# Optimization experiments

Measured on AMD Instinct MI355X. Metric: run time of the kernel, lower is better.

Reference implementation:

```python
import jax, jax.numpy as jnp
import numpy as np

B, T, V, H = 64, 101, 8000, 512
P_DROP = 0.3
EPS = 1e-5


def setup_inputs() -> dict:
    key = jax.random.key(0)
    ks = jax.random.split(key, 20)
    s = 1.0 / np.sqrt(H)
    inp = {
        "x": jax.random.randint(ks[0], (B, T), 0, V),
        "emb": jax.random.normal(ks[1], (V, H), jnp.float32) * 0.1,
        "Wd": jax.random.normal(ks[2], (V, H), jnp.float32) * s,
        "bd": jnp.zeros((V,), jnp.float32),
    }
    for l in range(1, 4):
        k = jax.random.split(ks[2 + l], 4)
        inp[f"Wih{l}"] = jax.random.normal(k[0], (4 * H, H), jnp.float32) * s
        inp[f"Whh{l}"] = jax.random.normal(k[1], (4 * H, H), jnp.float32) * s
        inp[f"b{l}"] = jnp.zeros((4 * H,), jnp.float32)
        inp[f"gamma{l}"] = jnp.ones((H,), jnp.float32)
        inp[f"beta{l}"] = jnp.zeros((H,), jnp.float32)
        # LockedDropout: one mask per sequence, reused at every timestep
        keep = jax.random.bernoulli(k[2], 1.0 - P_DROP, (B, H))
        inp[f"mask{l}"] = keep.astype(jnp.float32) / (1.0 - P_DROP)
    return inp


def _lstm_cell(x, h, c, Wih, Whh, b):
    gates = x @ Wih.T + h @ Whh.T + b  # [B, 4H]
    i, f, g, o = jnp.split(gates, 4, axis=-1)
    c = jax.nn.sigmoid(f) * c + jax.nn.sigmoid(i) * jnp.tanh(g)
    h = jax.nn.sigmoid(o) * jnp.tanh(c)
    return h, c


def _bn_train(h, gamma, beta):
    mu = jnp.mean(h, axis=0)
    var = jnp.mean(jnp.square(h - mu), axis=0)  # biased, as BatchNorm1d train
    return gamma * (h - mu) * jax.lax.rsqrt(var + EPS) + beta


def reference(x, emb, Wd, bd,
              Wih1, Whh1, b1, gamma1, beta1, mask1,
              Wih2, Whh2, b2, gamma2, beta2, mask2,
              Wih3, Whh3, b3, gamma3, beta3, mask3):
    e = emb[x]                      # [B, T, H]
    xs = jnp.swapaxes(e[:, :-1, :], 0, 1)  # [T-1, B, H]
    z = jnp.zeros((B, H), jnp.float32)

    def step(carry, xt):
        h1, c1, h2, c2, h3, c3 = carry
        h1, c1 = _lstm_cell(xt, h1, c1, Wih1, Whh1, b1)
        h = _bn_train(h1, gamma1, beta1) * mask1
        h2, c2 = _lstm_cell(h, h2, c2, Wih2, Whh2, b2)
        h = _bn_train(h2, gamma2, beta2) * mask2
        h3, c3 = _lstm_cell(h, h3, c3, Wih3, Whh3, b3)
        h = _bn_train(h3, gamma3, beta3) * mask3
        logits = h @ Wd.T + bd      # [B, V]
        return (h1, c1, h2, c2, h3, c3), logits

    _, logits = jax.lax.scan(step, (z, z, z, z, z, z), xs)  # [T-1, B, V]

    target_prediction = jnp.swapaxes(logits, 0, 1).reshape(-1, V)  # [B*(T-1), V]
    target = x[:, 1:].reshape(-1)
    logp = jax.nn.log_softmax(target_prediction, axis=-1)
    loss = -jnp.mean(jnp.take_along_axis(logp, target[:, None], axis=1))
    outputs = jnp.transpose(logits, (1, 2, 0))  # [B, V, T-1]
    return loss, outputs
```

## Files before the change

kernel.cpp:

```cpp
#include <hip/hip_runtime.h>
#include <hip/hip_bf16.h>
#include <math.h>

#define NBATCH 64
#define TT 101
#define TM 100
#define VV 8000
#define HH 512
#define H4 2048
#define EPSBN 1e-5f

typedef __attribute__((ext_vector_type(8))) short short8;
typedef __attribute__((ext_vector_type(4))) float floatx4;
typedef unsigned short bfraw;

__device__ __forceinline__ bfraw f2b(float f) {
  __hip_bfloat16 h = __float2bfloat16(f);
  return __builtin_bit_cast(bfraw, h);
}
__device__ __forceinline__ float sigm(float x) { return 1.f / (1.f + expf(-x)); }

__device__ __forceinline__ void st_u32_coh(bfraw* p, unsigned v) {
  __hip_atomic_store((unsigned*)p, v, __ATOMIC_RELAXED, __HIP_MEMORY_SCOPE_AGENT);
}
__device__ __forceinline__ void wait_ge(unsigned* p, unsigned target) {
  while (__hip_atomic_load(p, __ATOMIC_RELAXED, __HIP_MEMORY_SCOPE_AGENT) < target)
    __builtin_amdgcn_s_sleep(2);
}
__device__ __forceinline__ void wait_both(unsigned* p1, unsigned n1,
                                          unsigned* p2, unsigned n2) {
  for (;;) {
    unsigned a = __hip_atomic_load(p1, __ATOMIC_RELAXED, __HIP_MEMORY_SCOPE_AGENT);
    unsigned b = __hip_atomic_load(p2, __ATOMIC_RELAXED, __HIP_MEMORY_SCOPE_AGENT);
    if (a >= n1 && b >= n2) break;
    __builtin_amdgcn_s_sleep(2);
  }
}

#define GLD4(dst, base, OFFS) \
  asm volatile("global_load_dwordx4 %0, %1, off offset:" OFFS " sc1" \
               : "=&v"(dst) : "v"(base))
#define LD16(a, base) do { \
  GLD4(a[0],  base, "0");   GLD4(a[1],  base, "64");  \
  GLD4(a[2],  base, "128"); GLD4(a[3],  base, "192"); \
  GLD4(a[4],  base, "256"); GLD4(a[5],  base, "320"); \
  GLD4(a[6],  base, "384"); GLD4(a[7],  base, "448"); \
  GLD4(a[8],  base, "512"); GLD4(a[9],  base, "576"); \
  GLD4(a[10], base, "640"); GLD4(a[11], base, "704"); \
  GLD4(a[12], base, "768"); GLD4(a[13], base, "832"); \
  GLD4(a[14], base, "896"); GLD4(a[15], base, "960"); \
} while (0)

#define OFF_XE    0UL
#define OFF_X1    6553600UL
#define OFF_W1I   58982400UL
#define OFF_W1H   61079552UL
#define OFF_W2I   63176704UL
#define OFF_W2H   65273856UL
#define OFF_W3I   67371008UL
#define OFF_W3H   69468160UL
#define OFF_WDB   71565312UL
#define OFF_OUT1  79757312UL
#define OFF_OUT2  86310912UL
#define OFF_H3O   92864512UL
#define OFF_HST   99418112UL
#define OFF_ODONE 99811328UL
#define OFF_CST   100204544UL
#define OFF_SYNC  100597760UL
#define OFF_DONE  100597824UL
#define OFF_PMAX  100599040UL
#define OFF_PSUM  103799040UL
#define OFF_TLG   106999040UL

__global__ void k_zero(unsigned* p, int n) {
  int i = blockIdx.x * 256 + threadIdx.x;
  if (i < n) p[i] = 0u;
}

__global__ void k_embed(const int* __restrict__ x, const float* __restrict__ emb,
                        bfraw* __restrict__ xe) {
  int t = blockIdx.x >> 6, b = blockIdx.x & 63;
  int idx = x[b * TT + t];
  const float* src = emb + (size_t)idx * HH;
  bfraw* dst = xe + (size_t)blockIdx.x * HH;
  for (int e = threadIdx.x; e < HH; e += 256) dst[e] = f2b(src[e]);
}

__global__ void k_cast(const float* __restrict__ s, bfraw* __restrict__ d, int n) {
  int i = blockIdx.x * 256 + threadIdx.x;
  if (i < n) d[i] = f2b(s[i]);
}

__global__ __launch_bounds__(256) void k_gemm_x1(const bfraw* __restrict__ A,
                                                 const bfraw* __restrict__ Bw,
                                                 const float* __restrict__ bias,
                                                 float* __restrict__ X1) {
  int nb = blockIdx.x, mb = blockIdx.y;
  int tid = threadIdx.x, lane = tid & 63, wv = tid >> 6;
  int l15 = lane & 15, lq = lane >> 4;
  int m0 = mb * 64, n0 = nb * 64;
  floatx4 acc[4];
  for (int nt = 0; nt < 4; nt++) {
    float bv = bias[n0 + nt * 16 + l15];
    floatx4 t = {bv, bv, bv, bv};
    acc[nt] = t;
  }
  int arow = m0 + wv * 16 + l15;
  for (int ks = 0; ks < 16; ++ks) {
    int k = ks * 32 + lq * 8;
    short8 a = *(const short8*)&A[(size_t)arow * HH + k];
#pragma unroll
    for (int nt = 0; nt < 4; nt++) {
      short8 b = *(const short8*)&Bw[(size_t)(n0 + nt * 16 + l15) * HH + k];
      acc[nt] = __builtin_amdgcn_mfma_f32_16x16x32_bf16(a, b, acc[nt], 0, 0, 0);
    }
  }
#pragma unroll
  for (int nt = 0; nt < 4; nt++)
#pragma unroll
    for (int q = 0; q < 4; q++) {
      int m = m0 + wv * 16 + lq * 4 + q;
      X1[(size_t)m * H4 + n0 + nt * 16 + l15] = acc[nt][q];
    }
}

__global__ __launch_bounds__(256, 1) void k_recurrent(
    const float* __restrict__ X1,
    const bfraw* __restrict__ w1h, const bfraw* __restrict__ w2i, const bfraw* __restrict__ w2h,
    const bfraw* __restrict__ w3i, const bfraw* __restrict__ w3h,
    const float* __restrict__ b2, const float* __restrict__ b3,
    const float* __restrict__ g1, const float* __restrict__ be1, const float* __restrict__ mk1,
    const float* __restrict__ g2, const float* __restrict__ be2, const float* __restrict__ mk2,
    const float* __restrict__ g3, const float* __restrict__ be3, const float* __restrict__ mk3,
    bfraw* __restrict__ out1, bfraw* __restrict__ out2, bfraw* __restrict__ h3out,
    bfraw* __restrict__ hst, float* __restrict__ cst,
    unsigned* hdone, unsigned* odone) {
  __shared__ __align__(16) bfraw wlds[64 * 520];
  __shared__ __align__(16) float gd[64 * 65];
  __shared__ float stats[32];

  const int bid = blockIdx.x, tid = threadIdx.x;
  const int lane = tid & 63, wv = tid >> 6;
  const int l15 = lane & 15, lq = lane >> 4;

  int layer, cshift, j0;
  if (bid < 32)       { layer = 0; cshift = 4; j0 = bid << 4; }
  else if (bid < 96)  { layer = 1; cshift = 3; j0 = (bid - 32) << 3; }
  else                { layer = 2; cshift = 3; j0 = (bid - 96) << 3; }
  const int cols = 1 << cshift;
  const int NT = (layer == 0) ? 4 : 2;
  const int gstride = 4 * cols + 1;

  const bfraw* wih = (layer == 1) ? w2i : w3i;
  const bfraw* whh = (layer == 0) ? w1h : ((layer == 1) ? w2h : w3h);

  if (layer == 0) {
    for (int r = wv * 16; r < wv * 16 + 16; ++r) {
      int g = r >> 4, jj = r & 15;
      const bfraw* src = whh + (size_t)(g * HH + j0 + jj) * HH;
      *(short8*)&wlds[r * 520 + lane * 8] = *(const short8*)&src[lane * 8];
    }
  } else {
    for (int r2 = wv * 16; r2 < wv * 16 + 16; ++r2) {
      int mat = r2 >> 5, r = r2 & 31;
      int g = r >> 3, jj = r & 7;
      const bfraw* src = (mat ? whh : wih) + (size_t)(g * HH + j0 + jj) * HH;
      *(short8*)&wlds[r2 * 520 + lane * 8] = *(const short8*)&src[lane * 8];
    }
  }
  __syncthreads();

  const float* bb  = (layer == 1) ? b2 : b3;
  const float* gam = (layer == 0) ? g1 : ((layer == 1) ? g2 : g3);
  const float* bet = (layer == 0) ? be1 : ((layer == 1) ? be2 : be3);
  const float* msk = (layer == 0) ? mk1 : ((layer == 1) ? mk2 : mk3);
  bfraw* hbase = hst + (size_t)layer * 2 * NBATCH * HH;
  float* myc = cst + (size_t)layer * NBATCH * HH;

  const unsigned nprev = (layer == 1) ? 32u : 64u;
  const unsigned nself = (layer == 0) ? 32u : 64u;
  unsigned* oprev = odone + (layer - 1) * TM;
  unsigned* hself = hdone + layer * TM;
  unsigned* oself = odone + layer * TM;

  for (int t = 0; t < TM; ++t) {
    const bfraw* hr = hbase + (size_t)(t & 1) * NBATCH * HH;
    bfraw* hw = hbase + (size_t)((t + 1) & 1) * NBATCH * HH;
    const bfraw* xin = ((layer == 1) ? out1 : out2) + (size_t)t * NBATCH * HH;

    floatx4 acc[4];
    if (layer == 0) {
      const float* xrow = X1 + (size_t)t * NBATCH * H4;
      int rbase = wv * 16 + lq * 4;
#pragma unroll
      for (int nt = 0; nt < 4; nt++) {
        int colg = nt * HH + j0 + l15;
        acc[nt][0] = xrow[(rbase + 0) * H4 + colg];
        acc[nt][1] = xrow[(rbase + 1) * H4 + colg];
        acc[nt][2] = xrow[(rbase + 2) * H4 + colg];
        acc[nt][3] = xrow[(rbase + 3) * H4 + colg];
      }
    } else {
      floatx4 z = {0.f, 0.f, 0.f, 0.f};
      for (int nt = 0; nt < 4; nt++) acc[nt] = z;
    }

    if (tid == 0) {
      if (layer == 0) {
        if (t > 0) wait_ge(hself + t - 1, nself);
      } else {
        if (t > 0) wait_both(oprev + t, nprev, hself + t - 1, nself);
        else       wait_ge(oprev + t, nprev);
      }
    }
    __syncthreads();

    const int arow = wv * 16 + l15;
    const bfraw* ph = hr + (size_t)arow * HH + lq * 8;
    short8 hg[16];
    LD16(hg, ph);
    short8 xg[16];
    if (layer > 0) {
      const bfraw* px = xin + (size_t)arow * HH + lq * 8;
      LD16(xg, px);
    }
    asm volatile("s_waitcnt vmcnt(0)" ::: "memory");
    __builtin_amdgcn_sched_barrier(0);

    if (layer == 0) {
#pragma unroll
      for (int ks = 0; ks < 16; ++ks) {
        int k = ks * 32 + lq * 8;
#pragma unroll
        for (int nt = 0; nt < 4; nt++) {
          short8 bh = *(const short8*)&wlds[(nt * 16 + l15) * 520 + k];
          acc[nt] = __builtin_amdgcn_mfma_f32_16x16x32_bf16(hg[ks], bh, acc[nt], 0, 0, 0);
        }
      }
    } else {
#pragma unroll
      for (int ks = 0; ks < 16; ++ks) {
        int k = ks * 32 + lq * 8;
#pragma unroll
        for (int nt = 0; nt < 2; nt++) {
          short8 bx = *(const short8*)&wlds[(nt * 16 + l15) * 520 + k];
          short8 bh = *(const short8*)&wlds[((32 + nt * 16) + l15) * 520 + k];
          acc[nt] = __builtin_amdgcn_mfma_f32_16x16x32_bf16(xg[ks], bx, acc[nt], 0, 0, 0);
          acc[nt] = __builtin_amdgcn_mfma_f32_16x16x32_bf16(hg[ks], bh, acc[nt], 0, 0, 0);
        }
      }
    }
    {
      int rbase = wv * 16 + lq * 4;
      for (int nt = 0; nt < NT; nt++)
#pragma unroll
        for (int q = 0; q < 4; q++)
          gd[(rbase + q) * gstride + nt * 16 + l15] = acc[nt][q];
    }
    __syncthreads();
    const int half = cshift - 1;
    const int ne2 = NBATCH << half;
    for (int e = tid; e < ne2; e += 256) {
      int m = e >> half;
      int jp = (e & ((cols >> 1) - 1)) << 1;
      float hv[2];
#pragma unroll
      for (int u = 0; u < 2; u++) {
        int jj = jp + u, j = j0 + jj;
        float gi = gd[m * gstride + 0 * cols + jj];
        float gf = gd[m * gstride + 1 * cols + jj];
        float gg = gd[m * gstride + 2 * cols + jj];
        float go = gd[m * gstride + 3 * cols + jj];
        if (layer) { gi += bb[j]; gf += bb[HH + j]; gg += bb[2 * HH + j]; go += bb[3 * HH + j]; }
        float c = sigm(gf) * myc[m * HH + j] + sigm(gi) * tanhf(gg);
        float h = sigm(go) * tanhf(c);
        myc[m * HH + j] = c;
        hv[u] = h;
      }
      unsigned hpack = (unsigned)f2b(hv[0]) | ((unsigned)f2b(hv[1]) << 16);
      st_u32_coh(&hw[m * HH + j0 + jp], hpack);
      gd[m * gstride + jp] = hv[0];
      gd[m * gstride + jp + 1] = hv[1];
    }
    __builtin_amdgcn_s_waitcnt(0);
    __syncthreads();
    if (tid == 0)
      __hip_atomic_fetch_add(hself + t, 1u, __ATOMIC_RELAXED, __HIP_MEMORY_SCOPE_AGENT);
    {
      int tpc = 256 >> cshift;
      int c_ = tid >> (8 - cshift), r_ = tid & (tpc - 1);
      float s1 = 0.f, s2 = 0.f;
      for (int m = r_; m < NBATCH; m += tpc) {
        float v = gd[m * gstride + c_];
        s1 += v; s2 += v * v;
      }
      for (int off = 1; off < tpc; off <<= 1) {
        s1 += __shfl_xor(s1, off);
        s2 += __shfl_xor(s2, off);
      }
      if (r_ == 0) {
        float mu = s1 * (1.f / NBATCH);
        float var = s2 * (1.f / NBATCH) - mu * mu;
        stats[c_ * 2] = mu;
        stats[c_ * 2 + 1] = rsqrtf(var + EPSBN);
      }
    }
    __syncthreads();
    for (int e = tid; e < ne2; e += 256) {
      int m = e >> half;
      int jp = (e & ((cols >> 1) - 1)) << 1;
      float ov[2];
#pragma unroll
      for (int u = 0; u < 2; u++) {
        int jj = jp + u, j = j0 + jj;
        float h = gd[m * gstride + jj];
        ov[u] = (gam[j] * ((h - stats[jj * 2]) * stats[jj * 2 + 1]) + bet[j]) * msk[m * HH + j];
      }
      unsigned opack = (unsigned)f2b(ov[0]) | ((unsigned)f2b(ov[1]) << 16);
      if (layer == 0)
        st_u32_coh(&out1[(size_t)(t * NBATCH + m) * HH + j0 + jp], opack);
      else if (layer == 1)
        st_u32_coh(&out2[(size_t)(t * NBATCH + m) * HH + j0 + jp], opack);
      else
        *(unsigned*)&h3out[((size_t)m * TM + t) * HH + j0 + jp] = opack;
    }
    if (layer < 2) {
      __builtin_amdgcn_s_waitcnt(0);
      __syncthreads();
      if (tid == 0)
        __hip_atomic_fetch_add(oself + t, 1u, __ATOMIC_RELAXED, __HIP_MEMORY_SCOPE_AGENT);
    }
  }
}

__global__ __launch_bounds__(256) void k_dec(const bfraw* __restrict__ A,
                                             const bfraw* __restrict__ Bw,
                                             const float* __restrict__ bd,
                                             const int* __restrict__ x,
                                             float* __restrict__ out,
                                             float* __restrict__ pmax,
                                             float* __restrict__ psum,
                                             float* __restrict__ tlg) {
  __shared__ __align__(16) float tb[64 * 65];
  int nb = blockIdx.x, mb = blockIdx.y;
  int tid = threadIdx.x, lane = tid & 63, wv = tid >> 6;
  int l15 = lane & 15, lq = lane >> 4;
  int m0 = mb * 64, n0 = nb * 64;
  floatx4 acc[4];
  for (int nt = 0; nt < 4; nt++) {
    float bv = bd[n0 + nt * 16 + l15];
    floatx4 t = {bv, bv, bv, bv};
    acc[nt] = t;
  }
  int arow = m0 + wv * 16 + l15;
  for (int ks = 0; ks < 16; ++ks) {
    int k = ks * 32 + lq * 8;
    short8 a = *(const short8*)&A[(size_t)arow * HH + k];
#pragma unroll
    for (int nt = 0; nt < 4; nt++) {
      short8 b = *(const short8*)&Bw[(size_t)(n0 + nt * 16 + l15) * HH + k];
      acc[nt] = __builtin_amdgcn_mfma_f32_16x16x32_bf16(a, b, acc[nt], 0, 0, 0);
    }
  }
#pragma unroll
  for (int q = 0; q < 4; q++) {
    float mx = fmaxf(fmaxf(acc[0][q], acc[1][q]), fmaxf(acc[2][q], acc[3][q]));
    for (int off = 1; off < 16; off <<= 1) mx = fmaxf(mx, __shfl_xor(mx, off));
    float sm = expf(acc[0][q] - mx) + expf(acc[1][q] - mx) +
               expf(acc[2][q] - mx) + expf(acc[3][q] - mx);
    for (int off = 1; off < 16; off <<= 1) sm += __shfl_xor(sm, off);
    if (l15 == 0) {
      int m = m0 + wv * 16 + lq * 4 + q;
      pmax[(size_t)m * 125 + nb] = mx;
      psum[(size_t)m * 125 + nb] = sm;
    }
  }
  {
    int rbase = wv * 16 + lq * 4;
#pragma unroll
    for (int nt = 0; nt < 4; nt++)
#pragma unroll
      for (int q = 0; q < 4; q++)
        tb[(rbase + q) * 65 + nt * 16 + l15] = acc[nt][q];
  }
  __syncthreads();
  int ml = tid & 63, vq = tid >> 6;
  int m = m0 + ml;
  int b = m / TM, t = m - b * TM;
  int tgt = x[b * TT + t + 1];
  float* obase = out + (size_t)b * VV * TM + t;
  for (int i = 0; i < 16; ++i) {
    int cv = vq * 16 + i;
    int v = n0 + cv;
    float val = tb[ml * 65 + cv];
    obase[(size_t)v * TM] = val;
    if (v == tgt) tlg[m] = val;
  }
}

__global__ void k_loss(const float* __restrict__ pmax, const float* __restrict__ psum,
                       const float* __restrict__ tlg, float* acc) {
  int m = blockIdx.x * 4 + (threadIdx.x >> 6);
  int lane = threadIdx.x & 63;
  float mx = -3.4e38f;
  for (int i = lane; i < 125; i += 64) mx = fmaxf(mx, pmax[(size_t)m * 125 + i]);
  for (int off = 1; off < 64; off <<= 1) mx = fmaxf(mx, __shfl_xor(mx, off));
  float s = 0.f;
  for (int i = lane; i < 125; i += 64)
    s += psum[(size_t)m * 125 + i] * expf(pmax[(size_t)m * 125 + i] - mx);
  for (int off = 1; off < 64; off <<= 1) s += __shfl_xor(s, off);
  if (lane == 0) atomicAdd(acc, mx + logf(s) - tlg[m]);
}

__global__ void k_final(const float* acc, float* out) { out[0] = acc[0] * (1.f / 6400.f); }

extern "C" void kernel_launch(void* const* d_in, const int* in_sizes, int n_in,
                              void* d_out, int out_size, void* d_ws, size_t ws_size,
                              hipStream_t stream) {
  (void)in_sizes; (void)n_in; (void)out_size; (void)ws_size;
  const int*   x    = (const int*)  d_in[0];
  const float* emb  = (const float*)d_in[1];
  const float* Wd   = (const float*)d_in[2];
  const float* bd   = (const float*)d_in[3];
  const float* Wih1 = (const float*)d_in[4];
  const float* Whh1 = (const float*)d_in[5];
  const float* b1   = (const float*)d_in[6];
  const float* g1   = (const float*)d_in[7];
  const float* be1  = (const float*)d_in[8];
  const float* mk1  = (const float*)d_in[9];
  const float* Wih2 = (const float*)d_in[10];
  const float* Whh2 = (const float*)d_in[11];
  const float* b2   = (const float*)d_in[12];
  const float* g2   = (const float*)d_in[13];
  const float* be2  = (const float*)d_in[14];
  const float* mk2  = (const float*)d_in[15];
  const float* Wih3 = (const float*)d_in[16];
  const float* Whh3 = (const float*)d_in[17];
  const float* b3   = (const float*)d_in[18];
  const float* g3   = (const float*)d_in[19];
  const float* be3  = (const float*)d_in[20];
  const float* mk3  = (const float*)d_in[21];

  char* ws = (char*)d_ws;
  bfraw* XE   = (bfraw*)(ws + OFF_XE);
  float* X1   = (float*)(ws + OFF_X1);
  bfraw* W1I  = (bfraw*)(ws + OFF_W1I);
  bfraw* W1H  = (bfraw*)(ws + OFF_W1H);
  bfraw* W2I  = (bfraw*)(ws + OFF_W2I);
  bfraw* W2H  = (bfraw*)(ws + OFF_W2H);
  bfraw* W3I  = (bfraw*)(ws + OFF_W3I);
  bfraw* W3H  = (bfraw*)(ws + OFF_W3H);
  bfraw* WDB  = (bfraw*)(ws + OFF_WDB);
  bfraw* OUT1 = (bfraw*)(ws + OFF_OUT1);
  bfraw* OUT2 = (bfraw*)(ws + OFF_OUT2);
  bfraw* H3O  = (bfraw*)(ws + OFF_H3O);
  bfraw* HST  = (bfraw*)(ws + OFF_HST);
  float* CST  = (float*)(ws + OFF_CST);
  float* LACC = (float*)(ws + OFF_SYNC);
  unsigned* HDONE = (unsigned*)(ws + OFF_DONE);
  unsigned* ODONE = (unsigned*)(ws + OFF_ODONE);
  float* PMAX = (float*)(ws + OFF_PMAX);
  float* PSUM = (float*)(ws + OFF_PSUM);
  float* TLG  = (float*)(ws + OFF_TLG);

  int zwords = (int)((OFF_PMAX - OFF_HST) / 4);
  k_zero<<<(zwords + 255) / 256, 256, 0, stream>>>((unsigned*)(ws + OFF_HST), zwords);

  k_embed<<<6400, 256, 0, stream>>>(x, emb, XE);

  const int nw = H4 * HH;
  k_cast<<<(nw + 255) / 256, 256, 0, stream>>>(Wih1, W1I, nw);
  k_cast<<<(nw + 255) / 256, 256, 0, stream>>>(Whh1, W1H, nw);
  k_cast<<<(nw + 255) / 256, 256, 0, stream>>>(Wih2, W2I, nw);
  k_cast<<<(nw + 255) / 256, 256, 0, stream>>>(Whh2, W2H, nw);
  k_cast<<<(nw + 255) / 256, 256, 0, stream>>>(Wih3, W3I, nw);
  k_cast<<<(nw + 255) / 256, 256, 0, stream>>>(Whh3, W3H, nw);
  const int nwd = VV * HH;
  k_cast<<<(nwd + 255) / 256, 256, 0, stream>>>(Wd, WDB, nwd);

  k_gemm_x1<<<dim3(32, 100), 256, 0, stream>>>(XE, W1I, b1, X1);

  k_recurrent<<<160, 256, 0, stream>>>(X1, W1H, W2I, W2H, W3I, W3H, b2, b3,
                                       g1, be1, mk1, g2, be2, mk2, g3, be3, mk3,
                                       OUT1, OUT2, H3O, HST, CST, HDONE, ODONE);

  k_dec<<<dim3(125, 100), 256, 0, stream>>>(H3O, WDB, bd, x, ((float*)d_out) + 1,
                                            PMAX, PSUM, TLG);

  k_loss<<<1600, 256, 0, stream>>>(PMAX, PSUM, TLG, LACC);
  k_final<<<1, 1, 0, stream>>>(LACC, (float*)d_out);
}
```

Before: 1.831 ms.

## Use per-block ready flags and 32 blocks per layer in recurrent kernel

Layers 2 and 3 of the persistent recurrent kernel now use 32 blocks of 16 hidden columns each, like layer 1, instead of 64 blocks of 8. The grid drops from 160 to 96 blocks, and each block of those layers holds twice as many weight rows in LDS and runs twice the MFMA work. The shared atomic step counters are replaced by one flag per producer block per timestep, polled in parallel by 32 threads and combined with __syncthreads_and. The aim is to cut the number of blocks in each cross-block handoff and to avoid contended atomic adds on the critical path. The cost is heavier per-block compute, near-full LDS use, and an extra zeroing launch for the flag area, which reuses the embedding buffer.

```diff
diff --git a/kernel.cpp b/kernel.cpp
--- a/kernel.cpp
+++ b/kernel.cpp
@@ -23,18 +23,11 @@
 __device__ __forceinline__ void st_u32_coh(bfraw* p, unsigned v) {
   __hip_atomic_store((unsigned*)p, v, __ATOMIC_RELAXED, __HIP_MEMORY_SCOPE_AGENT);
 }
-__device__ __forceinline__ void wait_ge(unsigned* p, unsigned target) {
-  while (__hip_atomic_load(p, __ATOMIC_RELAXED, __HIP_MEMORY_SCOPE_AGENT) < target)
-    __builtin_amdgcn_s_sleep(2);
-}
-__device__ __forceinline__ void wait_both(unsigned* p1, unsigned n1,
-                                          unsigned* p2, unsigned n2) {
-  for (;;) {
-    unsigned a = __hip_atomic_load(p1, __ATOMIC_RELAXED, __HIP_MEMORY_SCOPE_AGENT);
-    unsigned b = __hip_atomic_load(p2, __ATOMIC_RELAXED, __HIP_MEMORY_SCOPE_AGENT);
-    if (a >= n1 && b >= n2) break;
-    __builtin_amdgcn_s_sleep(2);
-  }
+__device__ __forceinline__ unsigned ld_flag(const unsigned* p) {
+  return __hip_atomic_load(p, __ATOMIC_RELAXED, __HIP_MEMORY_SCOPE_AGENT);
+}
+__device__ __forceinline__ void st_flag(unsigned* p, unsigned v) {
+  __hip_atomic_store(p, v, __ATOMIC_RELAXED, __HIP_MEMORY_SCOPE_AGENT);
 }
 
 #define GLD4(dst, base, OFFS) \
@@ -51,6 +44,9 @@
   GLD4(a[14], base, "896"); GLD4(a[15], base, "960"); \
 } while (0)
 
+#define OFF_HFLG  0UL
+#define OFF_OFLG  153600UL
+#define FLG_BYTES 307200UL
 #define OFF_XE    0UL
 #define OFF_X1    6553600UL
 #define OFF_W1I   58982400UL
@@ -64,7 +60,6 @@
 #define OFF_OUT2  86310912UL
 #define OFF_H3O   92864512UL
 #define OFF_HST   99418112UL
-#define OFF_ODONE 99811328UL
 #define OFF_CST   100204544UL
 #define OFF_SYNC  100597760UL
 #define OFF_DONE  100597824UL
@@ -134,22 +129,16 @@
     const float* __restrict__ g3, const float* __restrict__ be3, const float* __restrict__ mk3,
     bfraw* __restrict__ out1, bfraw* __restrict__ out2, bfraw* __restrict__ h3out,
     bfraw* __restrict__ hst, float* __restrict__ cst,
-    unsigned* hdone, unsigned* odone) {
-  __shared__ __align__(16) bfraw wlds[64 * 520];
+    unsigned* hflag, unsigned* oflag) {
+  __shared__ __align__(16) bfraw wlds[128 * 520];
   __shared__ __align__(16) float gd[64 * 65];
   __shared__ float stats[32];
 
   const int bid = blockIdx.x, tid = threadIdx.x;
   const int lane = tid & 63, wv = tid >> 6;
   const int l15 = lane & 15, lq = lane >> 4;
-
-  int layer, cshift, j0;
-  if (bid < 32)       { layer = 0; cshift = 4; j0 = bid << 4; }
-  else if (bid < 96)  { layer = 1; cshift = 3; j0 = (bid - 32) << 3; }
-  else                { layer = 2; cshift = 3; j0 = (bid - 96) << 3; }
-  const int cols = 1 << cshift;
-  const int NT = (layer == 0) ? 4 : 2;
-  const int gstride = 4 * cols + 1;
+  const int layer = bid >> 5, myb = bid & 31;
+  const int j0 = myb << 4;
 
   const bfraw* wih = (layer == 1) ? w2i : w3i;
   const bfraw* whh = (layer == 0) ? w1h : ((layer == 1) ? w2h : w3h);
@@ -161,9 +150,9 @@
       *(short8*)&wlds[r * 520 + lane * 8] = *(const short8*)&src[lane * 8];
     }
   } else {
-    for (int r2 = wv * 16; r2 < wv * 16 + 16; ++r2) {
-      int mat = r2 >> 5, r = r2 & 31;
-      int g = r >> 3, jj = r & 7;
+    for (int r2 = wv * 32; r2 < wv * 32 + 32; ++r2) {
+      int mat = r2 >> 6, r = r2 & 63;
+      int g = r >> 4, jj = r & 15;
       const bfraw* src = (mat ? whh : wih) + (size_t)(g * HH + j0 + jj) * HH;
       *(short8*)&wlds[r2 * 520 + lane * 8] = *(const short8*)&src[lane * 8];
     }
@@ -177,11 +166,9 @@
   bfraw* hbase = hst + (size_t)layer * 2 * NBATCH * HH;
   float* myc = cst + (size_t)layer * NBATCH * HH;
 
-  const unsigned nprev = (layer == 1) ? 32u : 64u;
-  const unsigned nself = (layer == 0) ? 32u : 64u;
-  unsigned* oprev = odone + (layer - 1) * TM;
-  unsigned* hself = hdone + layer * TM;
-  unsigned* oself = odone + layer * TM;
+  unsigned* hfbase = hflag + (size_t)layer * TM * 32 * 4;
+  unsigned* ofprev = oflag + (size_t)(layer - 1) * TM * 32 * 4;
+  unsigned* ofself = oflag + (size_t)layer * TM * 32 * 4;
 
   for (int t = 0; t < TM; ++t) {
     const bfraw* hr = hbase + (size_t)(t & 1) * NBATCH * HH;
@@ -205,15 +192,15 @@
       for (int nt = 0; nt < 4; nt++) acc[nt] = z;
     }
 
-    if (tid == 0) {
-      if (layer == 0) {
-        if (t > 0) wait_ge(hself + t - 1, nself);
-      } else {
-        if (t > 0) wait_both(oprev + t, nprev, hself + t - 1, nself);
-        else       wait_ge(oprev + t, nprev);
-      }
-    }
-    __syncthreads();
+    for (;;) {
+      int ok = 1;
+      if (t > 0 && tid < 32)
+        ok = (ld_flag(hfbase + ((size_t)(t - 1) * 32 + tid) * 4) != 0);
+      else if (layer > 0 && tid >= 64 && tid < 96)
+        ok = (ld_flag(ofprev + ((size_t)t * 32 + (tid - 64)) * 4) != 0);
+      if (__syncthreads_and(ok)) break;
+      __builtin_amdgcn_s_sleep(1);
+    }
 
     const int arow = wv * 16 + l15;
     const bfraw* ph = hr + (size_t)arow * HH + lq * 8;
@@ -242,9 +229,9 @@
       for (int ks = 0; ks < 16; ++ks) {
         int k = ks * 32 + lq * 8;
 #pragma unroll
-        for (int nt = 0; nt < 2; nt++) {
+        for (int nt = 0; nt < 4; nt++) {
           short8 bx = *(const short8*)&wlds[(nt * 16 + l15) * 520 + k];
-          short8 bh = *(const short8*)&wlds[((32 + nt * 16) + l15) * 520 + k];
+          short8 bh = *(const short8*)&wlds[((64 + nt * 16) + l15) * 520 + k];
           acc[nt] = __builtin_amdgcn_mfma_f32_16x16x32_bf16(xg[ks], bx, acc[nt], 0, 0, 0);
           acc[nt] = __builtin_amdgcn_mfma_f32_16x16x32_bf16(hg[ks], bh, acc[nt], 0, 0, 0);
         }
@@ -252,25 +239,24 @@
     }
     {
       int rbase = wv * 16 + lq * 4;
-      for (int nt = 0; nt < NT; nt++)
+#pragma unroll
+      for (int nt = 0; nt < 4; nt++)
 #pragma unroll
         for (int q = 0; q < 4; q++)
-          gd[(rbase + q) * gstride + nt * 16 + l15] = acc[nt][q];
+          gd[(rbase + q) * 65 + nt * 16 + l15] = acc[nt][q];
     }
     __syncthreads();
-    const int half = cshift - 1;
-    const int ne2 = NBATCH << half;
-    for (int e = tid; e < ne2; e += 256) {
-      int m = e >> half;
-      int jp = (e & ((cols >> 1) - 1)) << 1;
+    for (int e = tid; e < 512; e += 256) {
+      int m = e >> 3;
+      int jp = (e & 7) << 1;
       float hv[2];
 #pragma unroll
       for (int u = 0; u < 2; u++) {
         int jj = jp + u, j = j0 + jj;
-        float gi = gd[m * gstride + 0 * cols + jj];
-        float gf = gd[m * gstride + 1 * cols + jj];
-        float gg = gd[m * gstride + 2 * cols + jj];
-        float go = gd[m * gstride + 3 * cols + jj];
+        float gi = gd[m * 65 + 0 * 16 + jj];
+        float gf = gd[m * 65 + 1 * 16 + jj];
+        float gg = gd[m * 65 + 2 * 16 + jj];
+        float go = gd[m * 65 + 3 * 16 + jj];
         if (layer) { gi += bb[j]; gf += bb[HH + j]; gg += bb[2 * HH + j]; go += bb[3 * HH + j]; }
         float c = sigm(gf) * myc[m * HH + j] + sigm(gi) * tanhf(gg);
         float h = sigm(go) * tanhf(c);
@@ -279,22 +265,21 @@
       }
       unsigned hpack = (unsigned)f2b(hv[0]) | ((unsigned)f2b(hv[1]) << 16);
       st_u32_coh(&hw[m * HH + j0 + jp], hpack);
-      gd[m * gstride + jp] = hv[0];
-      gd[m * gstride + jp + 1] = hv[1];
+      gd[m * 65 + jp] = hv[0];
+      gd[m * 65 + jp + 1] = hv[1];
     }
     __builtin_amdgcn_s_waitcnt(0);
     __syncthreads();
     if (tid == 0)
-      __hip_atomic_fetch_add(hself + t, 1u, __ATOMIC_RELAXED, __HIP_MEMORY_SCOPE_AGENT);
+      st_flag(hfbase + ((size_t)t * 32 + myb) * 4, 1u);
     {
-      int tpc = 256 >> cshift;
-      int c_ = tid >> (8 - cshift), r_ = tid & (tpc - 1);
+      int c_ = tid >> 4, r_ = tid & 15;
       float s1 = 0.f, s2 = 0.f;
-      for (int m = r_; m < NBATCH; m += tpc) {
-        float v = gd[m * gstride + c_];
+      for (int m = r_; m < NBATCH; m += 16) {
+        float v = gd[m * 65 + c_];
         s1 += v; s2 += v * v;
       }
-      for (int off = 1; off < tpc; off <<= 1) {
+      for (int off = 1; off < 16; off <<= 1) {
         s1 += __shfl_xor(s1, off);
         s2 += __shfl_xor(s2, off);
       }
@@ -306,14 +291,14 @@
       }
     }
     __syncthreads();
-    for (int e = tid; e < ne2; e += 256) {
-      int m = e >> half;
-      int jp = (e & ((cols >> 1) - 1)) << 1;
+    for (int e = tid; e < 512; e += 256) {
+      int m = e >> 3;
+      int jp = (e & 7) << 1;
       float ov[2];
 #pragma unroll
       for (int u = 0; u < 2; u++) {
         int jj = jp + u, j = j0 + jj;
-        float h = gd[m * gstride + jj];
+        float h = gd[m * 65 + jj];
         ov[u] = (gam[j] * ((h - stats[jj * 2]) * stats[jj * 2 + 1]) + bet[j]) * msk[m * HH + j];
       }
       unsigned opack = (unsigned)f2b(ov[0]) | ((unsigned)f2b(ov[1]) << 16);
@@ -328,7 +313,7 @@
       __builtin_amdgcn_s_waitcnt(0);
       __syncthreads();
       if (tid == 0)
-        __hip_atomic_fetch_add(oself + t, 1u, __ATOMIC_RELAXED, __HIP_MEMORY_SCOPE_AGENT);
+        st_flag(ofself + ((size_t)t * 32 + myb) * 4, 1u);
     }
   }
 }
@@ -457,8 +442,8 @@
   bfraw* HST  = (bfraw*)(ws + OFF_HST);
   float* CST  = (float*)(ws + OFF_CST);
   float* LACC = (float*)(ws + OFF_SYNC);
-  unsigned* HDONE = (unsigned*)(ws + OFF_DONE);
-  unsigned* ODONE = (unsigned*)(ws + OFF_ODONE);
+  unsigned* HFLG = (unsigned*)(ws + OFF_HFLG);
+  unsigned* OFLG = (unsigned*)(ws + OFF_OFLG);
   float* PMAX = (float*)(ws + OFF_PMAX);
   float* PSUM = (float*)(ws + OFF_PSUM);
   float* TLG  = (float*)(ws + OFF_TLG);
@@ -480,9 +465,12 @@
 
   k_gemm_x1<<<dim3(32, 100), 256, 0, stream>>>(XE, W1I, b1, X1);
 
-  k_recurrent<<<160, 256, 0, stream>>>(X1, W1H, W2I, W2H, W3I, W3H, b2, b3,
-                                       g1, be1, mk1, g2, be2, mk2, g3, be3, mk3,
-                                       OUT1, OUT2, H3O, HST, CST, HDONE, ODONE);
+  int fwords = (int)(FLG_BYTES / 4);
+  k_zero<<<(fwords + 255) / 256, 256, 0, stream>>>((unsigned*)(ws + OFF_HFLG), fwords);
+
+  k_recurrent<<<96, 256, 0, stream>>>(X1, W1H, W2I, W2H, W3I, W3H, b2, b3,
+                                      g1, be1, mk1, g2, be2, mk2, g3, be3, mk3,
+                                      OUT1, OUT2, H3O, HST, CST, HFLG, OFLG);
 
   k_dec<<<dim3(125, 100), 256, 0, stream>>>(H3O, WDB, bd, x, ((float*)d_out) + 1,
                                             PMAX, PSUM, TLG);
```

Result: slower. 2.106 ms (+15.0%).
